# Kernel optimization log

Hardware: AMD Instinct MI355X
Metric: run time of the kernel (lower is better)

Reference implementation:

```python
import jax, jax.numpy as jnp
import numpy as np

N, E, D, H, DH, FF, C, L = 50000, 640000, 128, 8, 16, 256, 5, 6
EPS = 1e-5


def _bn(x, g, b):
    # training-mode BatchNorm1d over the node dimension
    m = jnp.mean(x, axis=0)
    v = jnp.var(x, axis=0)
    return (x - m) * jax.lax.rsqrt(v + EPS) * g + b


def _sparse_mha(x, src, dst, Wq, Wk, Wv, Wo):
    # edge-restricted multi-head attention: softmax over incoming edges per dst node
    q = (x @ Wq).reshape(N, H, DH)
    k = (x @ Wk).reshape(N, H, DH)
    v = (x @ Wv).reshape(N, H, DH)
    s = jnp.einsum('ehd,ehd->eh', q[dst], k[src]) * (1.0 / np.sqrt(DH))  # [E,H]
    smax = jax.ops.segment_max(s, dst, num_segments=N)
    smax = jnp.where(jnp.isfinite(smax), smax, 0.0)  # guard isolated nodes
    e = jnp.exp(s - smax[dst])
    den = jax.ops.segment_sum(e, dst, num_segments=N)
    alpha = e / jnp.where(den > 0, den, 1.0)[dst]
    out = jax.ops.segment_sum(alpha[:, :, None] * v[src], dst, num_segments=N)  # [N,H,DH]
    return out.reshape(N, D) @ Wo


def setup_inputs() -> dict:
    key = jax.random.key(0)
    ks = jax.random.split(key, 18)
    f = lambda k, shp, sc: (jax.random.normal(k, shp, jnp.float32) * sc)
    return {
        'x': jax.random.normal(ks[0], (N, D), jnp.float32),
        'edge_index': jax.random.randint(ks[1], (2, E), 0, N),
        'Wq': f(ks[2], (L, D, D), 0.08),
        'Wk': f(ks[3], (L, D, D), 0.08),
        'Wv': f(ks[4], (L, D, D), 0.08),
        'Wo': f(ks[5], (L, D, D), 0.08),
        'g1': jnp.ones((L, D), jnp.float32),
        'bn1': jnp.zeros((L, D), jnp.float32),
        'W1': f(ks[6], (L, D, FF), 0.08),
        'bf1': jnp.zeros((L, FF), jnp.float32),
        'W2': f(ks[7], (L, FF, D), 0.06),
        'bf2': jnp.zeros((L, D), jnp.float32),
        'g2': jnp.ones((L, D), jnp.float32),
        'bn2': jnp.zeros((L, D), jnp.float32),
        'Wp': f(ks[8], (D, C), 0.08),
        'bp': jnp.zeros((C,), jnp.float32),
    }


def reference(x, edge_index, Wq, Wk, Wv, Wo, g1, bn1, W1, bf1, W2, bf2, g2, bn2, Wp, bp):
    src, dst = edge_index[0], edge_index[1]
    for i in range(L):  # fixed small layer count
        res = x  # residual is Identity (num_input == num_output)
        a = _sparse_mha(x, src, dst, Wq[i], Wk[i], Wv[i], Wo[i])
        x = _bn(a + res, g1[i], bn1[i])
        h = jax.nn.relu(x @ W1[i] + bf1[i])  # leakiness=0 -> relu
        x = _bn(x + (h @ W2[i] + bf2[i]), g2[i], bn2[i])
    node_pred = x @ Wp + bp
    return node_pred
```

## Files before the change

### kernel.cpp

```cpp
#include <hip/hip_runtime.h>
#include <hip/hip_bf16.h>
#include <cstdio>

#define NN 50000
#define EE 640000
#define DD 128
#define HH 8
#define DH 16
#define FFD 256
#define CC 5
#define LL 6
#define EPSV 1e-5f

typedef __attribute__((ext_vector_type(8))) short bf16x8;
typedef __attribute__((ext_vector_type(8))) unsigned short ushort8;
typedef __attribute__((ext_vector_type(4))) float f32x4;

__device__ __forceinline__ float bfu2f(unsigned short u) {
  union { unsigned int i; float f; } x; x.i = ((unsigned int)u) << 16; return x.f;
}
__device__ __forceinline__ unsigned short f2bf(float f) {
  union { float f; unsigned int i; } x; x.f = f;
  unsigned int r = (x.i + 0x7fffu + ((x.i >> 16) & 1u)) >> 16;
  return (unsigned short)r;
}

__global__ void detect_kernel(const unsigned int* __restrict__ g1w, int* __restrict__ flag) {
  if (threadIdx.x == 0 && blockIdx.x == 0) *flag = (g1w[0] == 0x3F803F80u) ? 1 : 0;
}

struct ConvJobs { const void* in[8]; float* out[8]; int n[8]; };
__global__ __launch_bounds__(256) void convert_batch_kernel(ConvJobs jobs, const int* __restrict__ flag) {
  int b = blockIdx.x;
  const void* in = jobs.in[b];
  float* out = jobs.out[b];
  int n = jobs.n[b];
  int use_bf = *flag;
  for (int i = threadIdx.x; i < n; i += 256) {
    if (use_bf) out[i] = bfu2f(((const unsigned short*)in)[i]);
    else        out[i] = ((const float*)in)[i];
  }
}

__global__ __launch_bounds__(256) void to_bf16_kernel(const void* __restrict__ in,
                                                      unsigned short* __restrict__ out, int n,
                                                      const int* __restrict__ flag) {
  int i = blockIdx.x * blockDim.x + threadIdx.x;
  if (i >= n) return;
  if (*flag) out[i] = ((const unsigned short*)in)[i];
  else       out[i] = f2bf(((const float*)in)[i]);
}

__global__ __launch_bounds__(256) void t_qkv_kernel(const void* __restrict__ wq, const void* __restrict__ wk,
                                                    const void* __restrict__ wv,
                                                    unsigned short* __restrict__ qkvT,
                                                    const int* __restrict__ flag) {
  int k = blockIdx.x, which = blockIdx.y, l = blockIdx.z;
  const void* in = (which == 0) ? wq : (which == 1) ? wk : wv;
  size_t off = (size_t)l * DD * DD;
  unsigned short* out = qkvT + (size_t)l * 384 * DD + (size_t)which * DD * DD;
  int use_bf = *flag;
  for (int n = threadIdx.x; n < DD; n += 256) {
    unsigned short v;
    if (use_bf) v = ((const unsigned short*)in)[off + (size_t)k * DD + n];
    else        v = f2bf(((const float*)in)[off + (size_t)k * DD + n]);
    out[(size_t)n * DD + k] = v;
  }
}

__global__ __launch_bounds__(256) void t_w_kernel(const void* __restrict__ in,
                                                  unsigned short* __restrict__ out,
                                                  int K, int N, const int* __restrict__ flag) {
  int k = blockIdx.x, l = blockIdx.y;
  size_t off = (size_t)l * K * N;
  unsigned short* o = out + (size_t)l * K * N;
  int use_bf = *flag;
  for (int n = threadIdx.x; n < N; n += 256) {
    unsigned short v;
    if (use_bf) v = ((const unsigned short*)in)[off + (size_t)k * N + n];
    else        v = f2bf(((const float*)in)[off + (size_t)k * N + n]);
    o[(size_t)n * K + k] = v;
  }
}

__global__ __launch_bounds__(256) void zero_kernel(int* __restrict__ p, int n) {
  int i = blockIdx.x * blockDim.x + threadIdx.x;
  if (i < n) p[i] = 0;
}

__global__ __launch_bounds__(256) void count_kernel(const int* __restrict__ dst, int* __restrict__ counts) {
  int e = blockIdx.x * blockDim.x + threadIdx.x;
  if (e < EE) atomicAdd(&counts[dst[e]], 1);
}

__global__ __launch_bounds__(256) void scan1_kernel(const int* __restrict__ counts,
                                                    int* __restrict__ row_ptr, int* __restrict__ partials) {
  __shared__ int sh[256];
  int t = threadIdx.x;
  int i = blockIdx.x * 256 + t;
  int v = (i < NN) ? counts[i] : 0;
  sh[t] = v; __syncthreads();
#pragma unroll
  for (int off = 1; off < 256; off <<= 1) {
    int u = (t >= off) ? sh[t - off] : 0;
    __syncthreads();
    sh[t] += u;
    __syncthreads();
  }
  if (i < NN) row_ptr[i] = sh[t] - v;
  if (t == 255) partials[blockIdx.x] = sh[t];
}

__global__ __launch_bounds__(256) void scan2_kernel(int* __restrict__ partials, int nb) {
  __shared__ int sh[256];
  int t = threadIdx.x;
  int v = (t < nb) ? partials[t] : 0;
  sh[t] = v; __syncthreads();
#pragma unroll
  for (int off = 1; off < 256; off <<= 1) {
    int u = (t >= off) ? sh[t - off] : 0;
    __syncthreads();
    sh[t] += u;
    __syncthreads();
  }
  if (t < nb) partials[t] = sh[t] - v;
}

__global__ __launch_bounds__(256) void scan3_kernel(int* __restrict__ row_ptr, const int* __restrict__ partials) {
  int i = blockIdx.x * 256 + threadIdx.x;
  if (i < NN) row_ptr[i] += partials[blockIdx.x];
  if (i == 0) row_ptr[NN] = EE;
}

__global__ __launch_bounds__(256) void fill_kernel(const int* __restrict__ src, const int* __restrict__ dst,
                                                   const int* __restrict__ row_ptr, int* __restrict__ cursor,
                                                   int* __restrict__ csr_src) {
  int e = blockIdx.x * blockDim.x + threadIdx.x;
  if (e < EE) {
    int d = dst[e];
    int pos = row_ptr[d] + atomicAdd(&cursor[d], 1);
    csr_src[pos] = src[e];
  }
}

template<int K, bool RELU, bool HASBIAS, bool HASRES, bool OUTBF, bool STATS>
__global__ __launch_bounds__(256) void mfma_gemm(const unsigned short* __restrict__ A,
                                                 const unsigned short* __restrict__ BT,
                                                 const float* __restrict__ bias,
                                                 const unsigned short* __restrict__ resid,
                                                 void* __restrict__ C, float* __restrict__ stats,
                                                 int M, int ldc) {
  __shared__ float lsum[128];
  __shared__ float lsq[128];
  int tid = threadIdx.x;
  int lane = tid & 63, wave = tid >> 6;
  int m0 = blockIdx.x * 128 + (wave >> 1) * 64;
  int n0 = blockIdx.y * 128 + (wave & 1) * 64;
  int lm = lane & 15;
  int quad = lane >> 4;
  int kq = quad * 8;

  int rowA[4];
#pragma unroll
  for (int r = 0; r < 4; r++) {
    int rr = m0 + 16 * r + lm;
    rowA[r] = (rr < M) ? rr : (M - 1);
  }

  f32x4 acc[4][4];
#pragma unroll
  for (int r = 0; r < 4; r++)
#pragma unroll
    for (int c = 0; c < 4; c++) acc[r][c] = (f32x4){0.f, 0.f, 0.f, 0.f};

#pragma unroll
  for (int k0 = 0; k0 < K; k0 += 32) {
    bf16x8 a[4], b[4];
#pragma unroll
    for (int r = 0; r < 4; r++)
      a[r] = *(const bf16x8*)(A + (size_t)rowA[r] * K + k0 + kq);
#pragma unroll
    for (int c = 0; c < 4; c++)
      b[c] = *(const bf16x8*)(BT + (size_t)(n0 + 16 * c + lm) * K + k0 + kq);
#pragma unroll
    for (int r = 0; r < 4; r++)
#pragma unroll
      for (int c = 0; c < 4; c++)
        acc[r][c] = __builtin_amdgcn_mfma_f32_16x16x32_bf16(a[r], b[c], acc[r][c], 0, 0, 0);
  }

  if (STATS) {
    if (tid < 128) { lsum[tid] = 0.f; lsq[tid] = 0.f; }
    __syncthreads();
  }

#pragma unroll
  for (int c = 0; c < 4; c++) {
    int col = n0 + 16 * c + lm;
    float bv = HASBIAS ? bias[col] : 0.f;
    float ps = 0.f, pss = 0.f;
#pragma unroll
    for (int r = 0; r < 4; r++) {
#pragma unroll
      for (int reg = 0; reg < 4; reg++) {
        int row = m0 + 16 * r + quad * 4 + reg;
        if (row < M) {
          float o = acc[r][c][reg] + bv;
          if (HASRES) o += bfu2f(resid[(size_t)row * ldc + col]);
          if (RELU) o = fmaxf(o, 0.f);
          size_t idx = (size_t)row * ldc + col;
          if (OUTBF) ((unsigned short*)C)[idx] = f2bf(o);
          else       ((float*)C)[idx] = o;
          if (STATS) { ps += o; pss = fmaf(o, o, pss); }
        }
      }
    }
    if (STATS) {
      int bcol = (wave & 1) * 64 + 16 * c + lm;
      atomicAdd(&lsum[bcol], ps);
      atomicAdd(&lsq[bcol], pss);
    }
  }
  if (STATS) {
    __syncthreads();
    if (tid < 128) {
      atomicAdd(&stats[tid], lsum[tid]);
      atomicAdd(&stats[128 + tid], lsq[tid]);
    }
  }
}

__global__ __launch_bounds__(256) void attn_kernel(const unsigned short* __restrict__ qkv,
                                                   const int* __restrict__ row_ptr,
                                                   const int* __restrict__ csr_src,
                                                   unsigned short* __restrict__ t1) {
  int t = blockIdx.x * blockDim.x + threadIdx.x;
  if (t >= NN * HH) return;
  int n = t >> 3, h = t & 7;
  const unsigned short* qp = qkv + (size_t)n * 384 + h * 16;
  float qf[16];
  {
    bf16x8 q0 = *(const bf16x8*)qp;
    bf16x8 q1 = *(const bf16x8*)(qp + 8);
#pragma unroll
    for (int i = 0; i < 8; i++) { qf[i] = bfu2f((unsigned short)q0[i]); qf[8 + i] = bfu2f((unsigned short)q1[i]); }
  }
  float m = -3.0e38f, l = 0.f;
  float A[16];
#pragma unroll
  for (int i = 0; i < 16; i++) A[i] = 0.f;
  int e0 = row_ptr[n], e1 = row_ptr[n + 1];
  if (e0 < e1) {
    int s = csr_src[e0];
    const unsigned short* kp = qkv + (size_t)s * 384 + 128 + h * 16;
    bf16x8 k0 = *(const bf16x8*)kp;
    bf16x8 k1 = *(const bf16x8*)(kp + 8);
    bf16x8 v0 = *(const bf16x8*)(kp + 128);
    bf16x8 v1 = *(const bf16x8*)(kp + 136);
    for (int e = e0; e < e1; e++) {
      int sn = csr_src[(e + 1 < e1) ? e + 1 : e];
      const unsigned short* kpn = qkv + (size_t)sn * 384 + 128 + h * 16;
      bf16x8 nk0 = *(const bf16x8*)kpn;
      bf16x8 nk1 = *(const bf16x8*)(kpn + 8);
      bf16x8 nv0 = *(const bf16x8*)(kpn + 128);
      bf16x8 nv1 = *(const bf16x8*)(kpn + 136);

      float sc = 0.f;
#pragma unroll
      for (int i = 0; i < 8; i++) {
        sc += qf[i] * bfu2f((unsigned short)k0[i]);
        sc += qf[8 + i] * bfu2f((unsigned short)k1[i]);
      }
      sc *= 0.25f;
      float mn = fmaxf(m, sc);
      float cf = __expf(m - mn);
      float p  = __expf(sc - mn);
      l = l * cf + p;
#pragma unroll
      for (int i = 0; i < 8; i++) {
        A[i]     = A[i]     * cf + p * bfu2f((unsigned short)v0[i]);
        A[8 + i] = A[8 + i] * cf + p * bfu2f((unsigned short)v1[i]);
      }
      m = mn;
      k0 = nk0; k1 = nk1; v0 = nv0; v1 = nv1;
    }
  }
  float inv = (l > 0.f) ? 1.f / l : 0.f;
  ushort8 o0, o1;
#pragma unroll
  for (int i = 0; i < 8; i++) { o0[i] = f2bf(A[i] * inv); o1[i] = f2bf(A[8 + i] * inv); }
  unsigned short* op = t1 + (size_t)n * 128 + h * 16;
  *(ushort8*)op = o0;
  *(ushort8*)(op + 8) = o1;
}

__global__ void bn_finalize_kernel(float* __restrict__ stats,
                                   const float* __restrict__ g,
                                   const float* __restrict__ b,
                                   float* __restrict__ ss) {
  int c = threadIdx.x;
  if (c < 128) {
    float mean = stats[c] * (1.f / NN);
    float var  = stats[128 + c] * (1.f / NN) - mean * mean;
    var = fmaxf(var, 0.f);
    float sc = g[c] * rsqrtf(var + EPSV);
    float sh = b[c] - mean * sc;
    ss[c] = sc; ss[128 + c] = sh;
    stats[c] = 0.f; stats[128 + c] = 0.f;
  }
}

__global__ __launch_bounds__(256) void bn_apply_kernel(const float4* __restrict__ y4,
                                                       const float4* __restrict__ ss4,
                                                       ushort4* __restrict__ xb) {
  int i = blockIdx.x * blockDim.x + threadIdx.x;
  const int total = NN * (DD / 4);
  if (i >= total) return;
  int c4 = i & 31;
  float4 v = y4[i], sc = ss4[c4], sh = ss4[32 + c4];
  ushort4 o;
  o.x = f2bf(fmaf(v.x, sc.x, sh.x));
  o.y = f2bf(fmaf(v.y, sc.y, sh.y));
  o.z = f2bf(fmaf(v.z, sc.z, sh.z));
  o.w = f2bf(fmaf(v.w, sc.w, sh.w));
  xb[i] = o;
}

__global__ __launch_bounds__(256) void proj_kernel(const unsigned short* __restrict__ x,
                                                   const float* __restrict__ Wp,
                                                   const float* __restrict__ bp,
                                                   void* __restrict__ out,
                                                   const int* __restrict__ flag) {
  __shared__ float W[DD * CC];
  __shared__ float bias[CC];
  for (int i = threadIdx.x; i < DD * CC; i += 256) W[i] = Wp[i];
  if (threadIdx.x < CC) bias[threadIdx.x] = bp[threadIdx.x];
  __syncthreads();
  int n = blockIdx.x * blockDim.x + threadIdx.x;
  if (n >= NN) return;
  float acc[CC];
#pragma unroll
  for (int c = 0; c < CC; c++) acc[c] = bias[c];
  const ushort4* xp = (const ushort4*)(x + (size_t)n * DD);
#pragma unroll
  for (int k4 = 0; k4 < DD / 4; k4++) {
    ushort4 u = xp[k4];
    float a0 = bfu2f(u.x), a1 = bfu2f(u.y), a2 = bfu2f(u.z), a3 = bfu2f(u.w);
    const float* w = &W[k4 * 4 * CC];
#pragma unroll
    for (int c = 0; c < CC; c++)
      acc[c] += a0 * w[c] + a1 * w[CC + c] + a2 * w[2 * CC + c] + a3 * w[3 * CC + c];
  }
  if (*flag) {
    __hip_bfloat16* o16 = (__hip_bfloat16*)out;
#pragma unroll
    for (int c = 0; c < CC; c++) o16[(size_t)n * CC + c] = __float2bfloat16(acc[c]);
  } else {
    float* o32 = (float*)out;
#pragma unroll
    for (int c = 0; c < CC; c++) o32[(size_t)n * CC + c] = acc[c];
  }
}

extern "C" void kernel_launch(void* const* d_in, const int* in_sizes, int n_in,
                              void* d_out, int out_size, void* d_ws, size_t ws_size,
                              hipStream_t stream) {
  const int* ei = (const int*)d_in[1];

  char* p = (char*)d_ws;
  auto carve = [&](size_t bytes) { char* r = p; p += (bytes + 255) & ~(size_t)255; return (void*)r; };
  unsigned short* xb   = (unsigned short*)carve((size_t)NN * DD * 2);
  unsigned short* qkv  = (unsigned short*)carve((size_t)NN * 384 * 2);
  unsigned short* t1   = (unsigned short*)carve((size_t)NN * DD * 2);
  unsigned short* hbuf = (unsigned short*)carve((size_t)NN * FFD * 2);
  float* y             = (float*)carve((size_t)NN * DD * 4);
  float* stats = (float*)carve(256 * 4);
  float* ss    = (float*)carve(256 * 4);
  int* row_ptr = (int*)carve((size_t)(NN + 1) * 4);
  int* cursor  = (int*)carve((size_t)NN * 4);
  int* csr_src = (int*)carve((size_t)EE * 4);
  int* flag    = (int*)carve(256);
  int* partials = (int*)carve(256 * 4);
  unsigned short* qkvT = (unsigned short*)carve((size_t)LL * 384 * DD * 2);
  unsigned short* WoT  = (unsigned short*)carve((size_t)LL * DD * DD * 2);
  unsigned short* W1T  = (unsigned short*)carve((size_t)LL * FFD * DD * 2);
  unsigned short* W2T  = (unsigned short*)carve((size_t)LL * DD * FFD * 2);
  float* g1_f  = (float*)carve((size_t)LL * DD * 4);
  float* bn1_f = (float*)carve((size_t)LL * DD * 4);
  float* bf1_f = (float*)carve((size_t)LL * FFD * 4);
  float* bf2_f = (float*)carve((size_t)LL * DD * 4);
  float* g2_f  = (float*)carve((size_t)LL * DD * 4);
  float* bn2_f = (float*)carve((size_t)LL * DD * 4);
  float* Wp_f  = (float*)carve((size_t)DD * CC * 4);
  float* bp_f  = (float*)carve((size_t)CC * 4);
  size_t need = (size_t)(p - (char*)d_ws);
  if (need > ws_size) {
    fprintf(stderr, "kernel_launch: workspace too small: need %zu, have %zu\n", need, ws_size);
    return;
  }

  const int* src  = ei;
  const int* dstp = ei + EE;

  detect_kernel<<<1, 64, 0, stream>>>((const unsigned int*)d_in[6], flag);
  to_bf16_kernel<<<(NN * DD + 255) / 256, 256, 0, stream>>>(d_in[0], xb, NN * DD, flag);

  {
    ConvJobs j;
    j.in[0] = d_in[6];  j.out[0] = g1_f;  j.n[0] = LL * DD;
    j.in[1] = d_in[7];  j.out[1] = bn1_f; j.n[1] = LL * DD;
    j.in[2] = d_in[9];  j.out[2] = bf1_f; j.n[2] = LL * FFD;
    j.in[3] = d_in[11]; j.out[3] = bf2_f; j.n[3] = LL * DD;
    j.in[4] = d_in[12]; j.out[4] = g2_f;  j.n[4] = LL * DD;
    j.in[5] = d_in[13]; j.out[5] = bn2_f; j.n[5] = LL * DD;
    j.in[6] = d_in[14]; j.out[6] = Wp_f;  j.n[6] = DD * CC;
    j.in[7] = d_in[15]; j.out[7] = bp_f;  j.n[7] = CC;
    convert_batch_kernel<<<8, 256, 0, stream>>>(j, flag);
  }

  t_qkv_kernel<<<dim3(DD, 3, LL), 256, 0, stream>>>(d_in[2], d_in[3], d_in[4], qkvT, flag);
  t_w_kernel<<<dim3(DD, LL), 256, 0, stream>>>(d_in[5], WoT, DD, DD, flag);
  t_w_kernel<<<dim3(DD, LL), 256, 0, stream>>>(d_in[8], W1T, DD, FFD, flag);
  t_w_kernel<<<dim3(FFD, LL), 256, 0, stream>>>(d_in[10], W2T, FFD, DD, flag);

  zero_kernel<<<1, 256, 0, stream>>>((int*)stats, 256);

  const int NB = (NN + 255) / 256;
  zero_kernel<<<(NN + 255) / 256, 256, 0, stream>>>(cursor, NN);
  count_kernel<<<(EE + 255) / 256, 256, 0, stream>>>(dstp, cursor);
  scan1_kernel<<<NB, 256, 0, stream>>>(cursor, row_ptr, partials);
  scan2_kernel<<<1, 256, 0, stream>>>(partials, NB);
  scan3_kernel<<<NB, 256, 0, stream>>>(row_ptr, partials);
  zero_kernel<<<(NN + 255) / 256, 256, 0, stream>>>(cursor, NN);
  fill_kernel<<<(EE + 255) / 256, 256, 0, stream>>>(src, dstp, row_ptr, cursor, csr_src);

  const int gm = (NN + 127) / 128;
  for (int layer = 0; layer < LL; layer++) {
    const unsigned short* qkvT_l = qkvT + (size_t)layer * 384 * DD;
    const unsigned short* WoT_l  = WoT  + (size_t)layer * DD * DD;
    const unsigned short* W1T_l  = W1T  + (size_t)layer * FFD * DD;
    const unsigned short* W2T_l  = W2T  + (size_t)layer * DD * FFD;

    mfma_gemm<128, false, false, false, true, false><<<dim3(gm, 3), 256, 0, stream>>>(
        xb, qkvT_l, nullptr, nullptr, qkv, nullptr, NN, 384);
    attn_kernel<<<(NN * HH + 255) / 256, 256, 0, stream>>>(qkv, row_ptr, csr_src, t1);
    mfma_gemm<128, false, false, true, false, true><<<dim3(gm, 1), 256, 0, stream>>>(
        t1, WoT_l, nullptr, xb, y, stats, NN, 128);
    bn_finalize_kernel<<<1, 128, 0, stream>>>(stats, g1_f + (size_t)layer * DD, bn1_f + (size_t)layer * DD, ss);
    bn_apply_kernel<<<(NN * 32 + 255) / 256, 256, 0, stream>>>((const float4*)y, (const float4*)ss, (ushort4*)xb);

    mfma_gemm<128, true, true, false, true, false><<<dim3(gm, 2), 256, 0, stream>>>(
        xb, W1T_l, bf1_f + (size_t)layer * FFD, nullptr, hbuf, nullptr, NN, 256);
    mfma_gemm<256, false, true, true, false, true><<<dim3(gm, 1), 256, 0, stream>>>(
        hbuf, W2T_l, bf2_f + (size_t)layer * DD, xb, y, stats, NN, 128);
    bn_finalize_kernel<<<1, 128, 0, stream>>>(stats, g2_f + (size_t)layer * DD, bn2_f + (size_t)layer * DD, ss);
    bn_apply_kernel<<<(NN * 32 + 255) / 256, 256, 0, stream>>>((const float4*)y, (const float4*)ss, (ushort4*)xb);
  }

  proj_kernel<<<(NN + 255) / 256, 256, 0, stream>>>(xb, Wp_f, bp_f, d_out, flag);
}
```

Baseline: 1.454 ms.

## Shrink GEMM tiles, fuse BN finalize into apply, degree-sort attention nodes

The GEMM tile per block shrinks from 128x128 to 128x64 (each wave computes 32x64), doubling the grid to raise occupancy and parallelism. The BN finalize kernel is folded into the apply kernel: each block recomputes scale and shift from per-layer stats slots, which removes a launch per BN and the stats-reset step. Attention threads are reordered by in-degree bucket so that nodes in a wavefront have similar edge counts, reducing divergence. The costs are repeated B-tile loads across more blocks and a few extra preprocessing launches for the bucket sort.

```diff
diff --git a/kernel.cpp b/kernel.cpp
--- a/kernel.cpp
+++ b/kernel.cpp
@@ -143,6 +143,25 @@
   }
 }
 
+__global__ __launch_bounds__(256) void bucket_count_kernel(const int* __restrict__ counts, int* __restrict__ bcount) {
+  int n = blockIdx.x * 256 + threadIdx.x;
+  if (n < NN) {
+    int d = min(counts[n], 255);
+    atomicAdd(&bcount[d], 1);
+  }
+}
+
+__global__ __launch_bounds__(256) void bucket_scatter_kernel(const int* __restrict__ counts,
+                                                             const int* __restrict__ boff, int* __restrict__ bcur,
+                                                             int* __restrict__ order) {
+  int n = blockIdx.x * 256 + threadIdx.x;
+  if (n < NN) {
+    int d = min(counts[n], 255);
+    int pos = boff[d] + atomicAdd(&bcur[d], 1);
+    order[pos] = n;
+  }
+}
+
 template<int K, bool RELU, bool HASBIAS, bool HASRES, bool OUTBF, bool STATS>
 __global__ __launch_bounds__(256) void mfma_gemm(const unsigned short* __restrict__ A,
                                                  const unsigned short* __restrict__ BT,
@@ -150,47 +169,47 @@
                                                  const unsigned short* __restrict__ resid,
                                                  void* __restrict__ C, float* __restrict__ stats,
                                                  int M, int ldc) {
-  __shared__ float lsum[128];
-  __shared__ float lsq[128];
+  __shared__ float lsum[64];
+  __shared__ float lsq[64];
   int tid = threadIdx.x;
   int lane = tid & 63, wave = tid >> 6;
-  int m0 = blockIdx.x * 128 + (wave >> 1) * 64;
-  int n0 = blockIdx.y * 128 + (wave & 1) * 64;
+  int m0 = blockIdx.x * 128 + wave * 32;
+  int n0 = blockIdx.y * 64;
   int lm = lane & 15;
   int quad = lane >> 4;
   int kq = quad * 8;
 
-  int rowA[4];
-#pragma unroll
-  for (int r = 0; r < 4; r++) {
+  int rowA[2];
+#pragma unroll
+  for (int r = 0; r < 2; r++) {
     int rr = m0 + 16 * r + lm;
     rowA[r] = (rr < M) ? rr : (M - 1);
   }
 
-  f32x4 acc[4][4];
-#pragma unroll
-  for (int r = 0; r < 4; r++)
+  f32x4 acc[2][4];
+#pragma unroll
+  for (int r = 0; r < 2; r++)
 #pragma unroll
     for (int c = 0; c < 4; c++) acc[r][c] = (f32x4){0.f, 0.f, 0.f, 0.f};
 
 #pragma unroll
   for (int k0 = 0; k0 < K; k0 += 32) {
-    bf16x8 a[4], b[4];
-#pragma unroll
-    for (int r = 0; r < 4; r++)
+    bf16x8 a[2], b[4];
+#pragma unroll
+    for (int r = 0; r < 2; r++)
       a[r] = *(const bf16x8*)(A + (size_t)rowA[r] * K + k0 + kq);
 #pragma unroll
     for (int c = 0; c < 4; c++)
       b[c] = *(const bf16x8*)(BT + (size_t)(n0 + 16 * c + lm) * K + k0 + kq);
 #pragma unroll
-    for (int r = 0; r < 4; r++)
+    for (int r = 0; r < 2; r++)
 #pragma unroll
       for (int c = 0; c < 4; c++)
         acc[r][c] = __builtin_amdgcn_mfma_f32_16x16x32_bf16(a[r], b[c], acc[r][c], 0, 0, 0);
   }
 
   if (STATS) {
-    if (tid < 128) { lsum[tid] = 0.f; lsq[tid] = 0.f; }
+    if (tid < 64) { lsum[tid] = 0.f; lsq[tid] = 0.f; }
     __syncthreads();
   }
 
@@ -200,7 +219,7 @@
     float bv = HASBIAS ? bias[col] : 0.f;
     float ps = 0.f, pss = 0.f;
 #pragma unroll
-    for (int r = 0; r < 4; r++) {
+    for (int r = 0; r < 2; r++) {
 #pragma unroll
       for (int reg = 0; reg < 4; reg++) {
         int row = m0 + 16 * r + quad * 4 + reg;
@@ -216,16 +235,15 @@
       }
     }
     if (STATS) {
-      int bcol = (wave & 1) * 64 + 16 * c + lm;
-      atomicAdd(&lsum[bcol], ps);
-      atomicAdd(&lsq[bcol], pss);
+      atomicAdd(&lsum[16 * c + lm], ps);
+      atomicAdd(&lsq[16 * c + lm], pss);
     }
   }
   if (STATS) {
     __syncthreads();
-    if (tid < 128) {
-      atomicAdd(&stats[tid], lsum[tid]);
-      atomicAdd(&stats[128 + tid], lsq[tid]);
+    if (tid < 64) {
+      atomicAdd(&stats[n0 + tid], lsum[tid]);
+      atomicAdd(&stats[128 + n0 + tid], lsq[tid]);
     }
   }
 }
@@ -233,10 +251,11 @@
 __global__ __launch_bounds__(256) void attn_kernel(const unsigned short* __restrict__ qkv,
                                                    const int* __restrict__ row_ptr,
                                                    const int* __restrict__ csr_src,
+                                                   const int* __restrict__ order,
                                                    unsigned short* __restrict__ t1) {
   int t = blockIdx.x * blockDim.x + threadIdx.x;
   if (t >= NN * HH) return;
-  int n = t >> 3, h = t & 7;
+  int n = order[t >> 3], h = t & 7;
   const unsigned short* qp = qkv + (size_t)n * 384 + h * 16;
   float qf[16];
   {
@@ -294,35 +313,33 @@
   *(ushort8*)(op + 8) = o1;
 }
 
-__global__ void bn_finalize_kernel(float* __restrict__ stats,
-                                   const float* __restrict__ g,
-                                   const float* __restrict__ b,
-                                   float* __restrict__ ss) {
-  int c = threadIdx.x;
-  if (c < 128) {
-    float mean = stats[c] * (1.f / NN);
-    float var  = stats[128 + c] * (1.f / NN) - mean * mean;
+__global__ __launch_bounds__(256) void bn_apply_kernel(const float4* __restrict__ y4,
+                                                       const float* __restrict__ statsL,
+                                                       const float* __restrict__ g,
+                                                       const float* __restrict__ b,
+                                                       ushort4* __restrict__ xb) {
+  __shared__ float ssc[128];
+  __shared__ float ssh[128];
+  int t = threadIdx.x;
+  if (t < 128) {
+    float mean = statsL[t] * (1.f / NN);
+    float var  = statsL[128 + t] * (1.f / NN) - mean * mean;
     var = fmaxf(var, 0.f);
-    float sc = g[c] * rsqrtf(var + EPSV);
-    float sh = b[c] - mean * sc;
-    ss[c] = sc; ss[128 + c] = sh;
-    stats[c] = 0.f; stats[128 + c] = 0.f;
-  }
-}
-
-__global__ __launch_bounds__(256) void bn_apply_kernel(const float4* __restrict__ y4,
-                                                       const float4* __restrict__ ss4,
-                                                       ushort4* __restrict__ xb) {
-  int i = blockIdx.x * blockDim.x + threadIdx.x;
+    float sc = g[t] * rsqrtf(var + EPSV);
+    ssc[t] = sc;
+    ssh[t] = b[t] - mean * sc;
+  }
+  __syncthreads();
+  int i = blockIdx.x * 256 + t;
   const int total = NN * (DD / 4);
   if (i >= total) return;
-  int c4 = i & 31;
-  float4 v = y4[i], sc = ss4[c4], sh = ss4[32 + c4];
+  int c4 = (i & 31) * 4;
+  float4 v = y4[i];
   ushort4 o;
-  o.x = f2bf(fmaf(v.x, sc.x, sh.x));
-  o.y = f2bf(fmaf(v.y, sc.y, sh.y));
-  o.z = f2bf(fmaf(v.z, sc.z, sh.z));
-  o.w = f2bf(fmaf(v.w, sc.w, sh.w));
+  o.x = f2bf(fmaf(v.x, ssc[c4 + 0], ssh[c4 + 0]));
+  o.y = f2bf(fmaf(v.y, ssc[c4 + 1], ssh[c4 + 1]));
+  o.z = f2bf(fmaf(v.z, ssc[c4 + 2], ssh[c4 + 2]));
+  o.w = f2bf(fmaf(v.w, ssc[c4 + 3], ssh[c4 + 3]));
   xb[i] = o;
 }
 
@@ -374,13 +391,16 @@
   unsigned short* t1   = (unsigned short*)carve((size_t)NN * DD * 2);
   unsigned short* hbuf = (unsigned short*)carve((size_t)NN * FFD * 2);
   float* y             = (float*)carve((size_t)NN * DD * 4);
-  float* stats = (float*)carve(256 * 4);
-  float* ss    = (float*)carve(256 * 4);
+  float* stats = (float*)carve(12 * 256 * 4);
   int* row_ptr = (int*)carve((size_t)(NN + 1) * 4);
   int* cursor  = (int*)carve((size_t)NN * 4);
+  int* counts  = (int*)carve((size_t)NN * 4);
   int* csr_src = (int*)carve((size_t)EE * 4);
+  int* order   = (int*)carve((size_t)NN * 4);
   int* flag    = (int*)carve(256);
   int* partials = (int*)carve(256 * 4);
+  int* bcount  = (int*)carve(256 * 4);
+  int* bcur    = (int*)carve(256 * 4);
   unsigned short* qkvT = (unsigned short*)carve((size_t)LL * 384 * DD * 2);
   unsigned short* WoT  = (unsigned short*)carve((size_t)LL * DD * DD * 2);
   unsigned short* W1T  = (unsigned short*)carve((size_t)LL * FFD * DD * 2);
@@ -423,16 +443,22 @@
   t_w_kernel<<<dim3(DD, LL), 256, 0, stream>>>(d_in[8], W1T, DD, FFD, flag);
   t_w_kernel<<<dim3(FFD, LL), 256, 0, stream>>>(d_in[10], W2T, FFD, DD, flag);
 
-  zero_kernel<<<1, 256, 0, stream>>>((int*)stats, 256);
+  zero_kernel<<<12, 256, 0, stream>>>((int*)stats, 12 * 256);
+  zero_kernel<<<2, 256, 0, stream>>>(bcount, 512);
+  zero_kernel<<<1, 256, 0, stream>>>(bcur, 256);
+  zero_kernel<<<(NN + 255) / 256, 256, 0, stream>>>(counts, NN);
+  zero_kernel<<<(NN + 255) / 256, 256, 0, stream>>>(cursor, NN);
 
   const int NB = (NN + 255) / 256;
-  zero_kernel<<<(NN + 255) / 256, 256, 0, stream>>>(cursor, NN);
-  count_kernel<<<(EE + 255) / 256, 256, 0, stream>>>(dstp, cursor);
-  scan1_kernel<<<NB, 256, 0, stream>>>(cursor, row_ptr, partials);
+  count_kernel<<<(EE + 255) / 256, 256, 0, stream>>>(dstp, counts);
+  scan1_kernel<<<NB, 256, 0, stream>>>(counts, row_ptr, partials);
   scan2_kernel<<<1, 256, 0, stream>>>(partials, NB);
   scan3_kernel<<<NB, 256, 0, stream>>>(row_ptr, partials);
-  zero_kernel<<<(NN + 255) / 256, 256, 0, stream>>>(cursor, NN);
   fill_kernel<<<(EE + 255) / 256, 256, 0, stream>>>(src, dstp, row_ptr, cursor, csr_src);
+
+  bucket_count_kernel<<<NB, 256, 0, stream>>>(counts, bcount);
+  scan2_kernel<<<1, 256, 0, stream>>>(bcount, 256);
+  bucket_scatter_kernel<<<NB, 256, 0, stream>>>(counts, bcount, bcur, order);
 
   const int gm = (NN + 127) / 128;
   for (int layer = 0; layer < LL; layer++) {
@@ -440,21 +466,23 @@
     const unsigned short* WoT_l  = WoT  + (size_t)layer * DD * DD;
     const unsigned short* W1T_l  = W1T  + (size_t)layer * FFD * DD;
     const unsigned short* W2T_l  = W2T  + (size_t)layer * DD * FFD;
-
-    mfma_gemm<128, false, false, false, true, false><<<dim3(gm, 3), 256, 0, stream>>>(
+    float* st1 = stats + (size_t)(layer * 2 + 0) * 256;
+    float* st2 = stats + (size_t)(layer * 2 + 1) * 256;
+
+    mfma_gemm<128, false, false, false, true, false><<<dim3(gm, 6), 256, 0, stream>>>(
         xb, qkvT_l, nullptr, nullptr, qkv, nullptr, NN, 384);
-    attn_kernel<<<(NN * HH + 255) / 256, 256, 0, stream>>>(qkv, row_ptr, csr_src, t1);
-    mfma_gemm<128, false, false, true, false, true><<<dim3(gm, 1), 256, 0, stream>>>(
-        t1, WoT_l, nullptr, xb, y, stats, NN, 128);
-    bn_finalize_kernel<<<1, 128, 0, stream>>>(stats, g1_f + (size_t)layer * DD, bn1_f + (size_t)layer * DD, ss);
-    bn_apply_kernel<<<(NN * 32 + 255) / 256, 256, 0, stream>>>((const float4*)y, (const float4*)ss, (ushort4*)xb);
-
-    mfma_gemm<128, true, true, false, true, false><<<dim3(gm, 2), 256, 0, stream>>>(
+    attn_kernel<<<(NN * HH + 255) / 256, 256, 0, stream>>>(qkv, row_ptr, csr_src, order, t1);
+    mfma_gemm<128, false, false, true, false, true><<<dim3(gm, 2), 256, 0, stream>>>(
+        t1, WoT_l, nullptr, xb, y, st1, NN, 128);
+    bn_apply_kernel<<<(NN * 32 + 255) / 256, 256, 0, stream>>>(
+        (const float4*)y, st1, g1_f + (size_t)layer * DD, bn1_f + (size_t)layer * DD, (ushort4*)xb);
+
+    mfma_gemm<128, true, true, false, true, false><<<dim3(gm, 4), 256, 0, stream>>>(
         xb, W1T_l, bf1_f + (size_t)layer * FFD, nullptr, hbuf, nullptr, NN, 256);
-    mfma_gemm<256, false, true, true, false, true><<<dim3(gm, 1), 256, 0, stream>>>(
-        hbuf, W2T_l, bf2_f + (size_t)layer * DD, xb, y, stats, NN, 128);
-    bn_finalize_kernel<<<1, 128, 0, stream>>>(stats, g2_f + (size_t)layer * DD, bn2_f + (size_t)layer * DD, ss);
-    bn_apply_kernel<<<(NN * 32 + 255) / 256, 256, 0, stream>>>((const float4*)y, (const float4*)ss, (ushort4*)xb);
+    mfma_gemm<256, false, true, true, false, true><<<dim3(gm, 2), 256, 0, stream>>>(
+        hbuf, W2T_l, bf2_f + (size_t)layer * DD, xb, y, st2, NN, 128);
+    bn_apply_kernel<<<(NN * 32 + 255) / 256, 256, 0, stream>>>(
+        (const float4*)y, st2, g2_f + (size_t)layer * DD, bn2_f + (size_t)layer * DD, (ushort4*)xb);
   }
 
   proj_kernel<<<(NN + 255) / 256, 256, 0, stream>>>(xb, Wp_f, bp_f, d_out, flag);
```

New measurement: 1.807 ms. 24.3% more time.
